# Kernel optimization log

Hardware: AMD Instinct MI355X
Metric: run time of the kernel (lower is better)

The kernel has to match this reference:

```python
import jax, jax.numpy as jnp
import numpy as np

B, T, E, U, V = 32, 512, 256, 512, 32000


def _gru_dir(x_proj, mask, U_w, b_rec, reverse):
    """Masked Keras GRU (reset_after=True). x_proj: [B,T,3U] (x@W + b_in), mask: [B,T] bool.
    Masked steps copy previous state through (Keras masking semantics)."""
    def step(h, inp):
        xt, mt = inp  # [B,3U], [B]
        rec = jnp.dot(h, U_w) + b_rec  # [B,3U]
        xz, xr, xh = jnp.split(xt, 3, axis=-1)
        hz, hr, hh = jnp.split(rec, 3, axis=-1)
        z = jax.nn.sigmoid(xz + hz)
        r = jax.nn.sigmoid(xr + hr)
        cand = jnp.tanh(xh + r * hh)
        h_new = z * h + (1.0 - z) * cand
        h_out = jnp.where(mt[:, None], h_new, h)
        return h_out, h_out

    h0 = jnp.zeros((x_proj.shape[0], U_w.shape[0]), x_proj.dtype)
    xs = (jnp.swapaxes(x_proj, 0, 1), jnp.swapaxes(mask, 0, 1))  # time-major
    h_last, seq = jax.lax.scan(step, h0, xs, reverse=reverse)
    return jnp.swapaxes(seq, 0, 1), h_last  # [B,T,U], [B,U]


def setup_inputs() -> dict:
    key = jax.random.key(0)
    ks = jax.random.split(key, 8)
    s_in = 0.05
    return {
        "tokens": jax.random.randint(ks[0], (B, T), 0, V),
        "emb": jax.random.normal(ks[1], (V, E), jnp.float32) * s_in,
        "W_fw": jax.random.normal(ks[2], (E, 3 * U), jnp.float32) * s_in,
        "U_fw": jax.random.normal(ks[3], (U, 3 * U), jnp.float32) * s_in,
        "b_in_fw": jnp.zeros((3 * U,), jnp.float32),
        "b_rec_fw": jnp.zeros((3 * U,), jnp.float32),
        "W_bw": jax.random.normal(ks[4], (E, 3 * U), jnp.float32) * s_in,
        "U_bw": jax.random.normal(ks[5], (U, 3 * U), jnp.float32) * s_in,
        "b_in_bw": jnp.zeros((3 * U,), jnp.float32),
        "b_rec_bw": jnp.zeros((3 * U,), jnp.float32),
    }


def reference(tokens, emb, W_fw, U_fw, b_in_fw, b_rec_fw, W_bw, U_bw, b_in_bw, b_rec_bw):
    mask = tokens != 0  # mask_zero=True
    x = emb[tokens]  # [B,T,E]
    # Precompute the input projections once (big GEMM), scan only the recurrence.
    fw_seq, _ = _gru_dir(jnp.dot(x, W_fw) + b_in_fw, mask, U_fw, b_rec_fw, reverse=False)
    bw_seq, _ = _gru_dir(jnp.dot(x, W_bw) + b_in_bw, mask, U_bw, b_rec_bw, reverse=True)
    return jnp.concatenate([fw_seq, bw_seq], axis=-1)  # [B,T,2U], merge_mode='concat'
```

## Files before the change

### kernel.cpp

```cpp
#include <hip/hip_runtime.h>
#include <stdint.h>

#define B_ 32
#define T_ 512
#define E_ 256
#define U_ 512
#define N3U_ 1536

typedef __bf16 bf16_t;
typedef bf16_t bf16x8 __attribute__((ext_vector_type(8)));
typedef float f32x4 __attribute__((ext_vector_type(4)));
typedef unsigned int u32x4 __attribute__((ext_vector_type(4)));

__device__ __forceinline__ unsigned short f2bf(float x) {
    union { float f; unsigned int u; } v; v.f = x;
    return (unsigned short)((v.u + 0x7fffu + ((v.u >> 16) & 1u)) >> 16);
}
__device__ __forceinline__ float bf2f(unsigned short h) {
    union { unsigned int u; float f; } v; v.u = ((unsigned int)h) << 16;
    return v.f;
}
__device__ __forceinline__ float fsigmoid(float x) {
    return 1.f / (1.f + __expf(-x));
}
__device__ __forceinline__ float ftanh(float x) {
    float ax = fabsf(x);
    float e  = __expf(-2.f * ax);
    float t  = (1.f - e) / (1.f + e);
    return copysignf(t, x);
}

__global__ __launch_bounds__(256) void gemm_xproj(
    const int* __restrict__ tokens, const float* __restrict__ emb,
    const float* __restrict__ Wf, const float* __restrict__ Wb,
    const float* __restrict__ binf, const float* __restrict__ binb,
    unsigned short* __restrict__ xpf, unsigned short* __restrict__ xpb)
{
    const int dir = blockIdx.z;
    const float* W   = dir ? Wb   : Wf;
    const float* bin = dir ? binb : binf;
    unsigned short* xp = dir ? xpb : xpf;

    const int n0 = blockIdx.x << 6;
    const int m0 = blockIdx.y << 6;
    const int tid  = threadIdx.x;
    const int lane = tid & 63;
    const int w    = tid >> 6;

    __shared__ __align__(16) unsigned short Ash[64][136];
    __shared__ __align__(16) unsigned short Bsh[64][136];

    f32x4 acc[4];
    for (int f = 0; f < 4; ++f) acc[f] = (f32x4){0.f, 0.f, 0.f, 0.f};

    for (int kt = 0; kt < 2; ++kt) {
        const int kbase = kt << 7;
        for (int p = 0; p < 8; ++p) {
            int row = (p << 3) + (tid >> 5);
            int c   = tid & 31;
            int tok = tokens[m0 + row];
            float4 v = *(const float4*)&emb[tok * E_ + kbase + (c << 2)];
            ushort4 o;
            o.x = f2bf(v.x); o.y = f2bf(v.y); o.z = f2bf(v.z); o.w = f2bf(v.w);
            *(ushort4*)&Ash[row][c << 2] = o;
        }
        for (int p = 0; p < 8; ++p) {
            int kl = (p << 4) + (tid >> 4);
            int j4 = (tid & 15) << 2;
            float4 v = *(const float4*)&W[(kbase + kl) * N3U_ + n0 + j4];
            Bsh[j4 + 0][kl] = f2bf(v.x);
            Bsh[j4 + 1][kl] = f2bf(v.y);
            Bsh[j4 + 2][kl] = f2bf(v.z);
            Bsh[j4 + 3][kl] = f2bf(v.w);
        }
        __syncthreads();
        for (int ks = 0; ks < 4; ++ks) {
            int off = (ks << 5) + ((lane >> 4) << 3);
            bf16x8 a = *(const bf16x8*)&Ash[(w << 4) + (lane & 15)][off];
            for (int f = 0; f < 4; ++f) {
                bf16x8 b = *(const bf16x8*)&Bsh[(f << 4) + (lane & 15)][off];
                acc[f] = __builtin_amdgcn_mfma_f32_16x16x32_bf16(a, b, acc[f], 0, 0, 0);
            }
        }
        __syncthreads();
    }
    const int col_l = lane & 15;
    const int mrow  = (w << 4) + ((lane >> 4) << 2);
    for (int f = 0; f < 4; ++f) {
        int col = n0 + (f << 4) + col_l;
        float bb = bin[col];
        for (int r = 0; r < 4; ++r) {
            int m = m0 + mrow + r;
            xp[m * N3U_ + col] = f2bf(acc[f][r] + bb);
        }
    }
}

#define RED(wc, g, wk, row, col) (((((wc)*3 + (g))*4 + (wk))*16 + (row))*18 + (col))
__global__ __launch_bounds__(512, 2) void gru_scan(
    const unsigned short* __restrict__ xpf, const unsigned short* __restrict__ xpb,
    const float* __restrict__ Uf, const float* __restrict__ Ub,
    const float* __restrict__ brf, const float* __restrict__ brb,
    const int* __restrict__ tokens,
    unsigned int* __restrict__ dat,
    unsigned int* __restrict__ sent,
    float* __restrict__ out)
{
    const int bx  = blockIdx.x;
    const int us  = bx & 15;
    const int mg  = (bx >> 4) & 1;
    const int dir = bx >> 5;
    const int u0  = us << 5;
    const int tid  = threadIdx.x;
    const int lane = tid & 63;
    const int w    = tid >> 6;
    const int wk   = w & 3;
    const int wc   = w >> 2;
    const int group = (dir << 1) | mg;

    const unsigned short* xp = dir ? xpb : xpf;
    const float* Uw = dir ? Ub : Uf;
    const float* br = dir ? brb : brf;

    __shared__ __align__(16) unsigned short Ahi[16][520];
    __shared__ __align__(16) unsigned short Alo[16][520];
    __shared__ __align__(16) float red[2 * 3 * 4 * 16 * 18];

    bf16x8 wfrag[4][3];
    const int quad = lane >> 4, nl = lane & 15;
    for (int ks = 0; ks < 4; ++ks)
        for (int g = 0; g < 3; ++g) {
            union { bf16x8 v; unsigned short s[8]; } uu;
            for (int j = 0; j < 8; ++j) {
                int k   = (wk << 7) + (ks << 5) + (quad << 3) + j;
                int col = (g << 9) + u0 + (wc << 4) + nl;
                uu.s[j] = f2bf(Uw[k * N3U_ + col]);
            }
            wfrag[ks][g] = uu.v;
        }

    const int bl = tid >> 5;
    const int cl = tid & 31;
    const int ewc = cl >> 4, ec16 = cl & 15;
    const int bg = (mg << 4) + bl;
    const int ug = u0 + cl;
    float hreg = 0.f;
    const float brz = br[ug], brr = br[512 + ug], brh = br[1024 + ug];

    const int lrow0 = tid >> 7;
    const int lcol4 = (tid & 127) << 2;
    const int spoll = (group << 8) + ((tid & 15) << 4);
    const int sown  = (group << 8) + (us << 4);

    for (int s = 0; s < T_; ++s) {
        const int t    = dir ? (T_ - 1 - s) : s;
        const int bufr = s & 1, bufw = bufr ^ 1;

        const int xrow = (bg * T_ + t) * N3U_;
        const unsigned short xzu = xp[xrow + ug];
        const unsigned short xru = xp[xrow + 512 + ug];
        const unsigned short xhu = xp[xrow + 1024 + ug];
        const int tok = tokens[bg * T_ + t];

        {
            unsigned int sv = __hip_atomic_load(&sent[spoll],
                                __ATOMIC_RELAXED, __HIP_MEMORY_SCOPE_AGENT);
            while (sv < (unsigned int)s) {
                __builtin_amdgcn_s_sleep(1);
                sv = __hip_atomic_load(&sent[spoll],
                        __ATOMIC_RELAXED, __HIP_MEMORY_SCOPE_AGENT);
            }
        }
        __syncthreads();

        const int dbase_r = (((bufr << 1) + dir) << 1 | mg) << 13;
        u32x4 pv0, pv1, pv2, pv3;
        {
            const unsigned int* a0 = dat + dbase_r + ((lrow0 +  0) << 9) + lcol4;
            const unsigned int* a1 = dat + dbase_r + ((lrow0 +  4) << 9) + lcol4;
            const unsigned int* a2 = dat + dbase_r + ((lrow0 +  8) << 9) + lcol4;
            const unsigned int* a3 = dat + dbase_r + ((lrow0 + 12) << 9) + lcol4;
            asm volatile("global_load_dwordx4 %0, %1, off sc0 sc1" : "=v"(pv0) : "v"(a0) : "memory");
            asm volatile("global_load_dwordx4 %0, %1, off sc0 sc1" : "=v"(pv1) : "v"(a1) : "memory");
            asm volatile("global_load_dwordx4 %0, %1, off sc0 sc1" : "=v"(pv2) : "v"(a2) : "memory");
            asm volatile("global_load_dwordx4 %0, %1, off sc0 sc1" : "=v"(pv3) : "v"(a3) : "memory");
            asm volatile("s_waitcnt vmcnt(0)" ::: "memory");
            __builtin_amdgcn_sched_barrier(0);
        }
        {
            ushort4 h4, l4;
#define UNP(PV, ROWOFF)                                                        \
            h4.x = (unsigned short)(PV.x & 0xffffu); l4.x = (unsigned short)(PV.x >> 16); \
            h4.y = (unsigned short)(PV.y & 0xffffu); l4.y = (unsigned short)(PV.y >> 16); \
            h4.z = (unsigned short)(PV.z & 0xffffu); l4.z = (unsigned short)(PV.z >> 16); \
            h4.w = (unsigned short)(PV.w & 0xffffu); l4.w = (unsigned short)(PV.w >> 16); \
            *(ushort4*)&Ahi[lrow0 + ROWOFF][lcol4] = h4;                        \
            *(ushort4*)&Alo[lrow0 + ROWOFF][lcol4] = l4;
            UNP(pv0, 0) UNP(pv1, 4) UNP(pv2, 8) UNP(pv3, 12)
#undef UNP
        }
        __syncthreads();

        f32x4 acc[3];
        acc[0] = (f32x4){0.f,0.f,0.f,0.f};
        acc[1] = (f32x4){0.f,0.f,0.f,0.f};
        acc[2] = (f32x4){0.f,0.f,0.f,0.f};
        for (int ks = 0; ks < 4; ++ks) {
            int off = (wk << 7) + (ks << 5) + (quad << 3);
            bf16x8 ahi = *(const bf16x8*)&Ahi[nl][off];
            bf16x8 alo = *(const bf16x8*)&Alo[nl][off];
#pragma unroll
            for (int g = 0; g < 3; ++g) {
                acc[g] = __builtin_amdgcn_mfma_f32_16x16x32_bf16(ahi, wfrag[ks][g], acc[g], 0, 0, 0);
                acc[g] = __builtin_amdgcn_mfma_f32_16x16x32_bf16(alo, wfrag[ks][g], acc[g], 0, 0, 0);
            }
        }
#pragma unroll
        for (int g = 0; g < 3; ++g)
#pragma unroll
            for (int r = 0; r < 4; ++r)
                red[RED(wc, g, wk, (quad << 2) + r, nl)] = acc[g][r];
        __syncthreads();

        float rz = brz, rr = brr, rh = brh;
#pragma unroll
        for (int k4 = 0; k4 < 4; ++k4) {
            rz += red[RED(ewc, 0, k4, bl, ec16)];
            rr += red[RED(ewc, 1, k4, bl, ec16)];
            rh += red[RED(ewc, 2, k4, bl, ec16)];
        }
        float xz = bf2f(xzu), xr = bf2f(xru), xh = bf2f(xhu);
        float z    = fsigmoid(xz + rz);
        float rg   = fsigmoid(xr + rr);
        float cand = ftanh(xh + rg * rh);
        float hn   = z * hreg + (1.f - z) * cand;
        float ho   = (tok != 0) ? hn : hreg;
        hreg = ho;

        unsigned short hi = f2bf(ho);
        unsigned short lo = f2bf(ho - bf2f(hi));
        const int dbase_w = (((bufw << 1) + dir) << 1 | mg) << 13;
        __hip_atomic_store(&dat[dbase_w + (bl << 9) + ug],
                           ((unsigned int)lo << 16) | (unsigned int)hi,
                           __ATOMIC_RELAXED, __HIP_MEMORY_SCOPE_AGENT);
        asm volatile("s_waitcnt vmcnt(0)" ::: "memory");
        __syncthreads();
        if (tid == 0)
            __hip_atomic_store(&sent[sown], (unsigned int)(s + 1),
                               __ATOMIC_RELAXED, __HIP_MEMORY_SCOPE_AGENT);

        out[(bg * T_ + t) * 1024 + (dir << 9) + ug] = ho;
    }
}

extern "C" void kernel_launch(void* const* d_in, const int* in_sizes, int n_in,
                              void* d_out, int out_size, void* d_ws, size_t ws_size,
                              hipStream_t stream)
{
    const size_t XP_BYTES  = (size_t)B_ * T_ * N3U_ * 2;
    const size_t DAT_OFF   = 2 * XP_BYTES;
    const size_t DAT_BYTES = (size_t)2 * 2 * 2 * 16 * 512 * 4;
    const size_t SENT_OFF  = DAT_OFF + DAT_BYTES;
    const size_t SENT_BYTES = 4 * 16 * 64;
    const size_t NEED      = SENT_OFF + SENT_BYTES;
    if (ws_size < NEED) return;

    const int*   tokens = (const int*)d_in[0];
    const float* emb    = (const float*)d_in[1];
    const float* W_fw   = (const float*)d_in[2];
    const float* U_fw   = (const float*)d_in[3];
    const float* bin_fw = (const float*)d_in[4];
    const float* brc_fw = (const float*)d_in[5];
    const float* W_bw   = (const float*)d_in[6];
    const float* U_bw   = (const float*)d_in[7];
    const float* bin_bw = (const float*)d_in[8];
    const float* brc_bw = (const float*)d_in[9];

    char* ws = (char*)d_ws;
    unsigned short* xpf = (unsigned short*)ws;
    unsigned short* xpb = (unsigned short*)(ws + XP_BYTES);
    unsigned int*   dat  = (unsigned int*)(ws + DAT_OFF);
    unsigned int*   sent = (unsigned int*)(ws + SENT_OFF);
    float* outp = (float*)d_out;

    hipMemsetAsync(ws + DAT_OFF, 0, DAT_BYTES + SENT_BYTES, stream);

    gemm_xproj<<<dim3(24, 256, 2), dim3(256), 0, stream>>>(
        tokens, emb, W_fw, W_bw, bin_fw, bin_bw, xpf, xpb);

    void* args[] = { (void*)&xpf, (void*)&xpb, (void*)&U_fw, (void*)&U_bw,
                     (void*)&brc_fw, (void*)&brc_bw, (void*)&tokens,
                     (void*)&dat, (void*)&sent, (void*)&outp };
    hipLaunchCooperativeKernel((const void*)gru_scan, dim3(64), dim3(512), args, 0, stream);
}
```

Before: 1.912 ms.

## Replace flag-based inter-block sync with parity tags embedded in state words

Drops the separate per-block 'sent' counter and its poll/store handshake. Each state word now carries a parity tag bit in the low bit of its lo-bf16 half, and readers spin on the data itself until every tag matches the expected step parity. This removes a poll round-trip, two __syncthreads and a store-wait per timestep. In exchange it loses one mantissa bit of the lo correction term and relies on the memset pattern to initialise the tags.

```diff
diff --git a/kernel.cpp b/kernel.cpp
--- a/kernel.cpp
+++ b/kernel.cpp
@@ -97,13 +97,13 @@
 }
 
 #define RED(wc, g, wk, row, col) (((((wc)*3 + (g))*4 + (wk))*16 + (row))*18 + (col))
+#define TAGBAD4(PV, E16) ((((PV[0] ^ (E16)) | (PV[1] ^ (E16)) | (PV[2] ^ (E16)) | (PV[3] ^ (E16))) >> 16) & 1u)
 __global__ __launch_bounds__(512, 2) void gru_scan(
     const unsigned short* __restrict__ xpf, const unsigned short* __restrict__ xpb,
     const float* __restrict__ Uf, const float* __restrict__ Ub,
     const float* __restrict__ brf, const float* __restrict__ brb,
     const int* __restrict__ tokens,
     unsigned int* __restrict__ dat,
-    unsigned int* __restrict__ sent,
     float* __restrict__ out)
 {
     const int bx  = blockIdx.x;
@@ -116,7 +116,6 @@
     const int w    = tid >> 6;
     const int wk   = w & 3;
     const int wc   = w >> 2;
-    const int group = (dir << 1) | mg;
 
     const unsigned short* xp = dir ? xpb : xpf;
     const float* Uw = dir ? Ub : Uf;
@@ -149,12 +148,10 @@
 
     const int lrow0 = tid >> 7;
     const int lcol4 = (tid & 127) << 2;
-    const int spoll = (group << 8) + ((tid & 15) << 4);
-    const int sown  = (group << 8) + (us << 4);
 
     for (int s = 0; s < T_; ++s) {
         const int t    = dir ? (T_ - 1 - s) : s;
-        const int bufr = s & 1, bufw = bufr ^ 1;
+        const int bufr = s & 1;
 
         const int xrow = (bg * T_ + t) * N3U_;
         const unsigned short xzu = xp[xrow + ug];
@@ -162,38 +159,43 @@
         const unsigned short xhu = xp[xrow + 1024 + ug];
         const int tok = tokens[bg * T_ + t];
 
-        {
-            unsigned int sv = __hip_atomic_load(&sent[spoll],
-                                __ATOMIC_RELAXED, __HIP_MEMORY_SCOPE_AGENT);
-            while (sv < (unsigned int)s) {
-                __builtin_amdgcn_s_sleep(1);
-                sv = __hip_atomic_load(&sent[spoll],
-                        __ATOMIC_RELAXED, __HIP_MEMORY_SCOPE_AGENT);
-            }
-        }
-        __syncthreads();
-
         const int dbase_r = (((bufr << 1) + dir) << 1 | mg) << 13;
+        const unsigned int exp16 = (((unsigned int)s >> 1) & 1u) << 16;
+        const unsigned int* a0 = dat + dbase_r + ((lrow0 +  0) << 9) + lcol4;
+        const unsigned int* a1 = dat + dbase_r + ((lrow0 +  4) << 9) + lcol4;
+        const unsigned int* a2 = dat + dbase_r + ((lrow0 +  8) << 9) + lcol4;
+        const unsigned int* a3 = dat + dbase_r + ((lrow0 + 12) << 9) + lcol4;
         u32x4 pv0, pv1, pv2, pv3;
-        {
-            const unsigned int* a0 = dat + dbase_r + ((lrow0 +  0) << 9) + lcol4;
-            const unsigned int* a1 = dat + dbase_r + ((lrow0 +  4) << 9) + lcol4;
-            const unsigned int* a2 = dat + dbase_r + ((lrow0 +  8) << 9) + lcol4;
-            const unsigned int* a3 = dat + dbase_r + ((lrow0 + 12) << 9) + lcol4;
-            asm volatile("global_load_dwordx4 %0, %1, off sc0 sc1" : "=v"(pv0) : "v"(a0) : "memory");
-            asm volatile("global_load_dwordx4 %0, %1, off sc0 sc1" : "=v"(pv1) : "v"(a1) : "memory");
-            asm volatile("global_load_dwordx4 %0, %1, off sc0 sc1" : "=v"(pv2) : "v"(a2) : "memory");
-            asm volatile("global_load_dwordx4 %0, %1, off sc0 sc1" : "=v"(pv3) : "v"(a3) : "memory");
+        asm volatile("global_load_dwordx4 %0, %1, off sc0 sc1" : "=v"(pv0) : "v"(a0) : "memory");
+        asm volatile("global_load_dwordx4 %0, %1, off sc0 sc1" : "=v"(pv1) : "v"(a1) : "memory");
+        asm volatile("global_load_dwordx4 %0, %1, off sc0 sc1" : "=v"(pv2) : "v"(a2) : "memory");
+        asm volatile("global_load_dwordx4 %0, %1, off sc0 sc1" : "=v"(pv3) : "v"(a3) : "memory");
+        asm volatile("s_waitcnt vmcnt(0)" ::: "memory");
+        unsigned int bad0 = TAGBAD4(pv0, exp16);
+        unsigned int bad1 = TAGBAD4(pv1, exp16);
+        unsigned int bad2 = TAGBAD4(pv2, exp16);
+        unsigned int bad3 = TAGBAD4(pv3, exp16);
+        while (bad0 | bad1 | bad2 | bad3) {
+            __builtin_amdgcn_s_sleep(1);
+            if (bad0) asm volatile("global_load_dwordx4 %0, %1, off sc0 sc1" : "=v"(pv0) : "v"(a0) : "memory");
+            if (bad1) asm volatile("global_load_dwordx4 %0, %1, off sc0 sc1" : "=v"(pv1) : "v"(a1) : "memory");
+            if (bad2) asm volatile("global_load_dwordx4 %0, %1, off sc0 sc1" : "=v"(pv2) : "v"(a2) : "memory");
+            if (bad3) asm volatile("global_load_dwordx4 %0, %1, off sc0 sc1" : "=v"(pv3) : "v"(a3) : "memory");
             asm volatile("s_waitcnt vmcnt(0)" ::: "memory");
-            __builtin_amdgcn_sched_barrier(0);
-        }
+            bad0 = TAGBAD4(pv0, exp16);
+            bad1 = TAGBAD4(pv1, exp16);
+            bad2 = TAGBAD4(pv2, exp16);
+            bad3 = TAGBAD4(pv3, exp16);
+        }
+        __builtin_amdgcn_sched_barrier(0);
+
         {
             ushort4 h4, l4;
 #define UNP(PV, ROWOFF)                                                        \
-            h4.x = (unsigned short)(PV.x & 0xffffu); l4.x = (unsigned short)(PV.x >> 16); \
-            h4.y = (unsigned short)(PV.y & 0xffffu); l4.y = (unsigned short)(PV.y >> 16); \
-            h4.z = (unsigned short)(PV.z & 0xffffu); l4.z = (unsigned short)(PV.z >> 16); \
-            h4.w = (unsigned short)(PV.w & 0xffffu); l4.w = (unsigned short)(PV.w >> 16); \
+            h4.x = (unsigned short)(PV[0] & 0xffffu); l4.x = (unsigned short)(PV[0] >> 16); \
+            h4.y = (unsigned short)(PV[1] & 0xffffu); l4.y = (unsigned short)(PV[1] >> 16); \
+            h4.z = (unsigned short)(PV[2] & 0xffffu); l4.z = (unsigned short)(PV[2] >> 16); \
+            h4.w = (unsigned short)(PV[3] & 0xffffu); l4.w = (unsigned short)(PV[3] >> 16); \
             *(ushort4*)&Ahi[lrow0 + ROWOFF][lcol4] = h4;                        \
             *(ushort4*)&Alo[lrow0 + ROWOFF][lcol4] = l4;
             UNP(pv0, 0) UNP(pv1, 4) UNP(pv2, 8) UNP(pv3, 12)
@@ -239,15 +241,11 @@
 
         unsigned short hi = f2bf(ho);
         unsigned short lo = f2bf(ho - bf2f(hi));
-        const int dbase_w = (((bufw << 1) + dir) << 1 | mg) << 13;
-        __hip_atomic_store(&dat[dbase_w + (bl << 9) + ug],
-                           ((unsigned int)lo << 16) | (unsigned int)hi,
-                           __ATOMIC_RELAXED, __HIP_MEMORY_SCOPE_AGENT);
-        asm volatile("s_waitcnt vmcnt(0)" ::: "memory");
-        __syncthreads();
-        if (tid == 0)
-            __hip_atomic_store(&sent[sown], (unsigned int)(s + 1),
-                               __ATOMIC_RELAXED, __HIP_MEMORY_SCOPE_AGENT);
+        unsigned int wtag = ((unsigned int)(s + 1) >> 1) & 1u;
+        unsigned int pv   = ((((unsigned int)lo & 0xFFFEu) | wtag) << 16) | (unsigned int)hi;
+        const int dbase_w = ((((bufr ^ 1) << 1) + dir) << 1 | mg) << 13;
+        unsigned int* dp  = dat + dbase_w + (bl << 9) + ug;
+        asm volatile("global_store_dword %0, %1, off sc0 sc1" :: "v"(dp), "v"(pv) : "memory");
 
         out[(bg * T_ + t) * 1024 + (dir << 9) + ug] = ho;
     }
@@ -260,9 +258,7 @@
     const size_t XP_BYTES  = (size_t)B_ * T_ * N3U_ * 2;
     const size_t DAT_OFF   = 2 * XP_BYTES;
     const size_t DAT_BYTES = (size_t)2 * 2 * 2 * 16 * 512 * 4;
-    const size_t SENT_OFF  = DAT_OFF + DAT_BYTES;
-    const size_t SENT_BYTES = 4 * 16 * 64;
-    const size_t NEED      = SENT_OFF + SENT_BYTES;
+    const size_t NEED      = DAT_OFF + DAT_BYTES;
     if (ws_size < NEED) return;
 
     const int*   tokens = (const int*)d_in[0];
@@ -279,17 +275,17 @@
     char* ws = (char*)d_ws;
     unsigned short* xpf = (unsigned short*)ws;
     unsigned short* xpb = (unsigned short*)(ws + XP_BYTES);
-    unsigned int*   dat  = (unsigned int*)(ws + DAT_OFF);
-    unsigned int*   sent = (unsigned int*)(ws + SENT_OFF);
+    unsigned int*   dat = (unsigned int*)(ws + DAT_OFF);
     float* outp = (float*)d_out;
 
-    hipMemsetAsync(ws + DAT_OFF, 0, DAT_BYTES + SENT_BYTES, stream);
+    hipMemsetAsync(ws + DAT_OFF, 0x00, DAT_BYTES / 2, stream);
+    hipMemsetAsync(ws + DAT_OFF + DAT_BYTES / 2, 0x01, DAT_BYTES / 2, stream);
 
     gemm_xproj<<<dim3(24, 256, 2), dim3(256), 0, stream>>>(
         tokens, emb, W_fw, W_bw, bin_fw, bin_bw, xpf, xpb);
 
     void* args[] = { (void*)&xpf, (void*)&xpb, (void*)&U_fw, (void*)&U_bw,
                      (void*)&brc_fw, (void*)&brc_bw, (void*)&tokens,
-                     (void*)&dat, (void*)&sent, (void*)&outp };
+                     (void*)&dat, (void*)&outp };
     hipLaunchCooperativeKernel((const void*)gru_scan, dim3(64), dim3(512), args, 0, stream);
 }
```

New measurement: 1.785 ms. 6.7% less time.
